# Kernel optimization log

Hardware: AMD Instinct MI355X
Metric: run time of the kernel (lower is better)

The kernel has to match this reference:

```python
import jax, jax.numpy as jnp
import numpy as np

K = 32            # config.k: active latents per token (batch top-k)
THRESHOLD_LR = 0.01
B, S, F = 8, 256, 16384


def setup_inputs() -> dict:
    key = jax.random.key(0)
    k1, k2 = jax.random.split(key)
    x = jax.random.normal(k1, (B, S, F), dtype=jnp.float32)
    token_mask = jax.random.randint(k2, (B, S), 0, 2, dtype=jnp.int32)
    threshold = jnp.zeros((), dtype=jnp.float32)  # persistent EMA buffer, init 0.0
    return {"x": x, "token_mask": token_mask, "threshold": threshold}


def reference(x, token_mask, threshold):
    # Training path of BatchTopKActivationFunction.forward
    b, s, f = x.shape
    num_tokens = b * s
    k_total = K * num_tokens
    neg_min = jnp.finfo(x.dtype).min
    # mask out tokens: x[~token_mask] = finfo.min (so they never enter top-k)
    xm = jnp.where(token_mask.astype(bool)[:, :, None], x, neg_min)
    flat = xm.reshape(-1)                       # [b*s*f]
    vals, idx = jax.lax.top_k(flat, k_total)    # global top-k over flattened tensor
    # scatter relu'd top-k values back into a zero tensor
    result = jnp.zeros_like(flat).at[idx].set(jax.nn.relu(vals)).reshape(b, s, f)
    # EMA threshold update: min of strictly-positive selected values
    pos = vals > 0
    min_pos = jnp.min(jnp.where(pos, vals, jnp.inf))
    new_threshold = jnp.where(
        jnp.any(pos),
        (1.0 - THRESHOLD_LR) * threshold + THRESHOLD_LR * min_pos,
        threshold,
    )
    return result, new_threshold
```

## Files before the change

kernel.cpp:

```cpp
#include <hip/hip_runtime.h>

#define N_ELEMS  33554432
#define N4       8388608
#define N_TOKENS 2048
#define F4       4096
#define K_TOTAL  65536u
#define NBINS    4096

#define C_NG       4096
#define C_WINTH    4097
#define C_CANDTH   4098
#define C_NEED     4099
#define C_FB       4100
#define C_N2       4101
#define C_DONE     4102
#define N_CTR_END  4160

#define GLIST_OFF  8192u
#define CAPG       4194304u
#define LIST2_OFF  (GLIST_OFF + 2u*CAPG)
#define CAP2       4096u
#define FB1_OFF    16777216u
#define CAPF       2097152u
#define FB2_OFF    (FB1_OFF + 2u*CAPF)

#define GBUF 1024
#define GH_BLOCKS 32

__device__ __forceinline__ unsigned keyOf(float f) {
    unsigned b = __float_as_uint(f);
    return b ^ ((unsigned)((int)b >> 31) | 0x80000000u);
}
__device__ __forceinline__ float valOf(unsigned u) {
    unsigned b = (u & 0x80000000u) ? (u ^ 0x80000000u) : ~u;
    return __uint_as_float(b);
}
__device__ __forceinline__ unsigned umaxu(unsigned a, unsigned b) { return a > b ? a : b; }

__global__ void k_init(unsigned* __restrict__ ws) {
    int t = blockIdx.x * 256 + threadIdx.x;
    if (t < N_CTR_END) ws[t] = 0u;
}

__global__ __launch_bounds__(512) void k_stream(const float4* __restrict__ x,
                                                const int* __restrict__ mask,
                                                unsigned* __restrict__ ws,
                                                float4* __restrict__ out) {
    __shared__ uint2 sbuf[GBUF];
    __shared__ unsigned s_cnt, s_base;
    const int tok = blockIdx.x;
    const int tid = threadIdx.x;
    float4* ot = out + (size_t)tok * F4;
    const float4 z = make_float4(0.f, 0.f, 0.f, 0.f);
    if (!mask[tok]) {
        for (int j = tid; j < F4; j += 512) ot[j] = z;
        return;
    }
    if (tid == 0) s_cnt = 0u;
    __syncthreads();
    uint2* glist = (uint2*)(ws + GLIST_OFF);
    const float4* xt = x + (size_t)tok * F4;
    const unsigned baseIdx = (unsigned)tok * 16384u;
    #pragma unroll
    for (int half = 0; half < 2; ++half) {
        const int j0 = tid + half * 2048;
        float4 v0 = xt[j0];
        float4 v1 = xt[j0 + 512];
        float4 v2 = xt[j0 + 1024];
        float4 v3 = xt[j0 + 1536];
        ot[j0] = z; ot[j0 + 512] = z; ot[j0 + 1024] = z; ot[j0 + 1536] = z;
        float fv[16] = {v0.x, v0.y, v0.z, v0.w, v1.x, v1.y, v1.z, v1.w,
                        v2.x, v2.y, v2.z, v2.w, v3.x, v3.y, v3.z, v3.w};
        #pragma unroll
        for (int c = 0; c < 16; ++c) {
            float f = fv[c];
            if (f >= 2.0f) {
                unsigned u = keyOf(f);
                unsigned slot = atomicAdd(&s_cnt, 1u);
                unsigned j = (unsigned)(j0 + (c >> 2) * 512);
                uint2 e = make_uint2(u, baseIdx + j * 4u + (unsigned)(c & 3));
                if (slot < GBUF) sbuf[slot] = e;
                else { unsigned g = atomicAdd(&ws[C_NG], 1u); if (g < CAPG) glist[g] = e; }
            }
        }
    }
    __syncthreads();
    unsigned cnt = s_cnt; if (cnt > GBUF) cnt = GBUF;
    if (tid == 0) s_base = atomicAdd(&ws[C_NG], cnt);
    __syncthreads();
    for (unsigned j = tid; j < cnt; j += 512) {
        unsigned p = s_base + j;
        if (p < CAPG) glist[p] = sbuf[j];
    }
}

__global__ __launch_bounds__(1024) void k_ghist(unsigned* __restrict__ ws) {
    __shared__ unsigned lh[NBINS];
    __shared__ unsigned s_last, s_b1, s_ka, s_found;
    const int t = threadIdx.x;
    for (int b = t; b < NBINS; b += 1024) lh[b] = 0u;
    if (t == 0) s_last = 0u;
    __syncthreads();
    const unsigned ngRaw = ws[C_NG];
    unsigned ng = ngRaw > CAPG ? CAPG : ngRaw;
    const uint2* glist = (const uint2*)(ws + GLIST_OFF);
    for (unsigned i = blockIdx.x * 1024u + (unsigned)t; i < ng; i += GH_BLOCKS * 1024u) {
        unsigned u = glist[i].x;
        unsigned bin = (u - 0xC0000000u) >> 12;
        if (bin > 4095u) bin = 4095u;
        atomicAdd(&lh[bin], 1u);
    }
    __syncthreads();
    for (int b = t; b < NBINS; b += 1024) {
        unsigned c = lh[b];
        if (c) atomicAdd(&ws[b], c);
    }
    __syncthreads();
    if (t == 0) {
        __threadfence();
        unsigned done = atomicAdd(&ws[C_DONE], 1u) + 1u;
        if (done == GH_BLOCKS) s_last = 1u;
    }
    __syncthreads();
    if (!s_last) return;
    unsigned vv[4]; unsigned s = 0u;
    #pragma unroll
    for (int j = 0; j < 4; ++j) {
        vv[j] = __hip_atomic_load(&ws[t * 4 + j], __ATOMIC_RELAXED, __HIP_MEMORY_SCOPE_AGENT);
        s += vv[j];
    }
    unsigned* sc = lh;
    if (t == 0) s_found = 0u;
    sc[t] = s;
    __syncthreads();
    for (int off = 1; off < 1024; off <<= 1) {
        unsigned a = sc[t];
        unsigned b2 = (t + off < 1024) ? sc[t + off] : 0u;
        __syncthreads();
        sc[t] = a + b2;
        __syncthreads();
    }
    unsigned run = (t < 1023) ? sc[t + 1] : 0u;
    #pragma unroll
    for (int j = 3; j >= 0; --j) {
        unsigned prev = run; run += vv[j];
        if (run >= K_TOTAL && prev < K_TOTAL) {
            s_b1 = (unsigned)(t * 4 + j); s_ka = prev; s_found = 1u;
        }
    }
    __syncthreads();
    if (t == 0) {
        unsigned total = sc[0];
        unsigned fb = (s_found == 0u) || (total < K_TOTAL) || (s_b1 == 4095u) || (ngRaw > CAPG);
        ws[C_FB] = fb ? 1u : 0u;
        if (!fb) {
            unsigned candTh = 0xC0000000u + (s_b1 << 12);
            ws[C_CANDTH] = candTh;
            ws[C_WINTH]  = candTh + 0x1000u;
            ws[C_NEED]   = K_TOTAL - s_ka;
        }
    }
}

__global__ __launch_bounds__(256) void k_scatter(unsigned* __restrict__ ws,
                                                 float* __restrict__ out) {
    if (ws[C_FB]) return;
    const unsigned winTh = ws[C_WINTH], candTh = ws[C_CANDTH];
    unsigned ng = ws[C_NG]; if (ng > CAPG) ng = CAPG;
    uint2* glist = (uint2*)(ws + GLIST_OFF);
    uint2* list2 = (uint2*)(ws + LIST2_OFF);
    const unsigned stride = gridDim.x * 256u;
    for (unsigned i = blockIdx.x * 256u + (unsigned)threadIdx.x; i < ng; i += stride) {
        uint2 e = glist[i];
        if (e.x >= winTh) out[e.y] = valOf(e.x);
        else if (e.x >= candTh) {
            unsigned g = atomicAdd(&ws[C_N2], 1u);
            if (g < CAP2) list2[g] = e;
        }
    }
}

__global__ __launch_bounds__(1024) void k_tail(const float4* __restrict__ x,
                                               const int* __restrict__ mask,
                                               unsigned* __restrict__ ws,
                                               float* __restrict__ out,
                                               const float* __restrict__ thr) {
    __shared__ __align__(16) unsigned smem[9216];
    __shared__ unsigned sB1, sKA, sMode, sNegmin, sB2, sNeed, sCnt;
    const int t = threadIdx.x;
    const unsigned rawn2 = ws[C_N2];
    const unsigned fb = ws[C_FB] | (rawn2 > CAP2 ? 1u : 0u);

    if (!fb) {
        uint2* ent = (uint2*)smem;
        unsigned* red = smem + 8192;
        const unsigned n2 = rawn2;
        const unsigned need = ws[C_NEED];
        uint2* list2 = (uint2*)(ws + LIST2_OFF);
        for (unsigned i = (unsigned)t; i < n2; i += 1024u) ent[i] = list2[i];
        __syncthreads();
        unsigned minSel = 0xFFFFFFFFu;
        for (unsigned i = (unsigned)t; i < n2; i += 1024u) {
            uint2 e = ent[i];
            unsigned rank = 0u;
            for (unsigned j = 0; j < n2; ++j) {
                uint2 o = ent[j];
                rank += (o.x > e.x || (o.x == e.x && o.y < e.y)) ? 1u : 0u;
            }
            if (rank < need) {
                out[e.y] = valOf(e.x);
                if (e.x < minSel) minSel = e.x;
            }
        }
        red[t] = minSel;
        __syncthreads();
        for (int off = 512; off > 0; off >>= 1) {
            if (t < off) red[t] = red[t] < red[t + off] ? red[t] : red[t + off];
            __syncthreads();
        }
        if (t == 0) {
            out[N_ELEMS] = 0.99f * thr[0] + 0.01f * valOf(red[0]);
        }
        return;
    }

    unsigned* lh = smem;
    unsigned* sred = smem + 4096;
    for (int b = t; b < NBINS; b += 1024) lh[b] = 0u;
    if (t == 0) sCnt = 0u;
    __syncthreads();
    unsigned negmin = 0u;
    for (int tok = 0; tok < N_TOKENS; ++tok) {
        if (!mask[tok]) continue;
        const float4* xt = x + (size_t)tok * F4;
        for (int j = t; j < F4; j += 1024) {
            float4 v = xt[j];
            float fv[4] = {v.x, v.y, v.z, v.w};
            #pragma unroll
            for (int c = 0; c < 4; ++c) {
                float f = fv[c];
                unsigned u = keyOf(f);
                atomicAdd(&lh[u >> 20], 1u);
                if (f > 0.0f) negmin = umaxu(negmin, ~u);
            }
        }
    }
    __syncthreads();
    sred[t] = negmin; __syncthreads();
    for (int off = 512; off > 0; off >>= 1) {
        if (t < off) sred[t] = umaxu(sred[t], sred[t + off]);
        __syncthreads();
    }
    if (t == 0) {
        sNegmin = sred[0];
        unsigned tot = 0u;
        for (int b = 0; b < NBINS; ++b) tot += lh[b];
        if (tot <= K_TOTAL) sMode = 1u;
        else {
            sMode = 0u;
            unsigned run = 0u, prev = 0u; int b1 = 0;
            for (int b = NBINS - 1; b >= 0; --b) {
                prev = run; run += lh[b];
                if (run >= K_TOTAL && prev < K_TOTAL) { b1 = b; break; }
            }
            sB1 = (unsigned)b1; sKA = prev;
        }
        sCnt = 0u;
    }
    __syncthreads();
    if (sMode == 1u) {
        for (int tok = 0; tok < N_TOKENS; ++tok) {
            if (!mask[tok]) continue;
            const float4* xt = x + (size_t)tok * F4;
            float* ot = out + (size_t)tok * 16384;
            for (int j = t; j < F4; j += 1024) {
                float4 v = xt[j];
                ot[j * 4 + 0] = fmaxf(v.x, 0.f); ot[j * 4 + 1] = fmaxf(v.y, 0.f);
                ot[j * 4 + 2] = fmaxf(v.z, 0.f); ot[j * 4 + 3] = fmaxf(v.w, 0.f);
            }
        }
        if (t == 0) {
            float th = thr[0], newt = th;
            if (sNegmin) newt = 0.99f * th + 0.01f * valOf(~sNegmin);
            out[N_ELEMS] = newt;
        }
        return;
    }
    const unsigned B1c = sB1;
    uint2* fb1 = (uint2*)(ws + FB1_OFF);
    for (int tok = 0; tok < N_TOKENS; ++tok) {
        if (!mask[tok]) continue;
        const float4* xt = x + (size_t)tok * F4;
        const unsigned baseIdx = (unsigned)tok * 16384u;
        for (int j = t; j < F4; j += 1024) {
            float4 v = xt[j];
            float fv[4] = {v.x, v.y, v.z, v.w};
            #pragma unroll
            for (int c = 0; c < 4; ++c) {
                float f = fv[c];
                unsigned u = keyOf(f);
                unsigned p = u >> 20;
                unsigned idx = baseIdx + (unsigned)j * 4u + (unsigned)c;
                if (p > B1c) out[idx] = fmaxf(f, 0.f);
                else if (p == B1c) {
                    unsigned g = atomicAdd(&sCnt, 1u);
                    if (g < CAPF) fb1[g] = make_uint2(u, idx);
                }
            }
        }
    }
    __syncthreads();
    unsigned n1 = sCnt > CAPF ? CAPF : sCnt;
    __syncthreads();
    if (t < 256) lh[t] = 0u;
    if (t == 0) sCnt = 0u;
    __syncthreads();
    for (unsigned i = t; i < n1; i += 1024)
        atomicAdd(&lh[(fb1[i].x >> 12) & 255u], 1u);
    __syncthreads();
    if (t == 0) {
        unsigned run = sKA, prev = sKA; int b2 = 0;
        for (int b = 255; b >= 0; --b) {
            prev = run; run += lh[b];
            if (run >= K_TOTAL) { b2 = b; break; }
        }
        sB2 = (unsigned)b2; sNeed = K_TOTAL - prev;
    }
    __syncthreads();
    const unsigned B2 = sB2, need = sNeed;
    uint2* fb2 = (uint2*)(ws + FB2_OFF);
    for (unsigned i = t; i < n1; i += 1024) {
        uint2 e = fb1[i];
        unsigned bb = (e.x >> 12) & 255u;
        if (bb > B2) out[e.y] = fmaxf(valOf(e.x), 0.f);
        else if (bb == B2) {
            unsigned g = atomicAdd(&sCnt, 1u);
            if (g < CAPF) fb2[g] = e;
        }
    }
    __syncthreads();
    unsigned n2 = sCnt > CAPF ? CAPF : sCnt;
    unsigned minSel = 0xFFFFFFFFu;
    for (unsigned i = t; i < n2; i += 1024) {
        uint2 e = fb2[i];
        unsigned rank = 0u;
        for (unsigned jj = 0; jj < n2; ++jj) {
            uint2 o = fb2[jj];
            rank += (o.x > e.x || (o.x == e.x && o.y < e.y)) ? 1u : 0u;
        }
        if (rank < need) { out[e.y] = fmaxf(valOf(e.x), 0.f); if (e.x < minSel) minSel = e.x; }
    }
    __syncthreads();
    sred[t] = minSel; __syncthreads();
    for (int off = 512; off > 0; off >>= 1) {
        if (t < off) sred[t] = sred[t] < sred[t + off] ? sred[t] : sred[t + off];
        __syncthreads();
    }
    if (t == 0) {
        float th = thr[0], newt = th;
        unsigned vku = sred[0];
        if (vku != 0xFFFFFFFFu) {
            float vk = valOf(vku);
            float minpos; int any;
            if (vk > 0.f) { minpos = vk; any = 1; }
            else { any = (sNegmin != 0u); minpos = any ? valOf(~sNegmin) : 0.f; }
            if (any) newt = 0.99f * th + 0.01f * minpos;
        }
        out[N_ELEMS] = newt;
    }
}

extern "C" void kernel_launch(void* const* d_in, const int* in_sizes, int n_in,
                              void* d_out, int out_size, void* d_ws, size_t ws_size,
                              hipStream_t stream) {
    const float4* x  = (const float4*)d_in[0];
    const int* mask  = (const int*)d_in[1];
    const float* thr = (const float*)d_in[2];
    float* out       = (float*)d_out;
    unsigned* ws     = (unsigned*)d_ws;

    k_init    <<<17, 256, 0, stream>>>(ws);
    k_stream  <<<N_TOKENS, 512, 0, stream>>>(x, mask, ws, (float4*)out);
    k_ghist   <<<GH_BLOCKS, 1024, 0, stream>>>(ws);
    k_scatter <<<256, 256, 0, stream>>>(ws, out);
    k_tail    <<<1, 1024, 0, stream>>>(x, mask, ws, out, thr);
}
```

Baseline: 272.3 us.

## Defer output zeroing to per-token emit kernel using pivot threshold

The streaming pass now only gates candidates and records a per-token segment (base, count) in global memory instead of zeroing the output. A multi-block candidate kernel finds the exact pivot key and index with a last-block rank step. A new per-token emit kernel then zeroes each row and writes the selected values from its own segment, so the final scatter is local to each row rather than random across the whole output. Overflow of the shared buffer now forces the fallback path instead of spilling to the global list. The cost is an extra pass over the output rows and an extra kernel launch.

```diff
diff --git a/kernel.cpp b/kernel.cpp
--- a/kernel.cpp
+++ b/kernel.cpp
@@ -1,7 +1,6 @@
 #include <hip/hip_runtime.h>
 
 #define N_ELEMS  33554432
-#define N4       8388608
 #define N_TOKENS 2048
 #define F4       4096
 #define K_TOTAL  65536u
@@ -14,9 +13,13 @@
 #define C_FB       4100
 #define C_N2       4101
 #define C_DONE     4102
+#define C_PK       4107
+#define C_PIDX     4108
+#define C_DONE2    4109
 #define N_CTR_END  4160
 
-#define GLIST_OFF  8192u
+#define SEG_OFF    4608u
+#define GLIST_OFF  16384u
 #define CAPG       4194304u
 #define LIST2_OFF  (GLIST_OFF + 2u*CAPG)
 #define CAP2       4096u
@@ -26,6 +29,7 @@
 
 #define GBUF 1024
 #define GH_BLOCKS 32
+#define CP_BLOCKS 64
 
 __device__ __forceinline__ unsigned keyOf(float f) {
     unsigned b = __float_as_uint(f);
@@ -42,23 +46,19 @@
     if (t < N_CTR_END) ws[t] = 0u;
 }
 
-__global__ __launch_bounds__(512) void k_stream(const float4* __restrict__ x,
-                                                const int* __restrict__ mask,
-                                                unsigned* __restrict__ ws,
-                                                float4* __restrict__ out) {
+__global__ __launch_bounds__(512) void k_gate(const float4* __restrict__ x,
+                                              const int* __restrict__ mask,
+                                              unsigned* __restrict__ ws) {
     __shared__ uint2 sbuf[GBUF];
     __shared__ unsigned s_cnt, s_base;
     const int tok = blockIdx.x;
     const int tid = threadIdx.x;
-    float4* ot = out + (size_t)tok * F4;
-    const float4 z = make_float4(0.f, 0.f, 0.f, 0.f);
     if (!mask[tok]) {
-        for (int j = tid; j < F4; j += 512) ot[j] = z;
+        if (tid == 0) { ws[SEG_OFF + 2u*tok] = 0u; ws[SEG_OFF + 2u*tok + 1u] = 0u; }
         return;
     }
     if (tid == 0) s_cnt = 0u;
     __syncthreads();
-    uint2* glist = (uint2*)(ws + GLIST_OFF);
     const float4* xt = x + (size_t)tok * F4;
     const unsigned baseIdx = (unsigned)tok * 16384u;
     #pragma unroll
@@ -68,7 +68,6 @@
         float4 v1 = xt[j0 + 512];
         float4 v2 = xt[j0 + 1024];
         float4 v3 = xt[j0 + 1536];
-        ot[j0] = z; ot[j0 + 512] = z; ot[j0 + 1024] = z; ot[j0 + 1536] = z;
         float fv[16] = {v0.x, v0.y, v0.z, v0.w, v1.x, v1.y, v1.z, v1.w,
                         v2.x, v2.y, v2.z, v2.w, v3.x, v3.y, v3.z, v3.w};
         #pragma unroll
@@ -78,18 +77,26 @@
                 unsigned u = keyOf(f);
                 unsigned slot = atomicAdd(&s_cnt, 1u);
                 unsigned j = (unsigned)(j0 + (c >> 2) * 512);
-                uint2 e = make_uint2(u, baseIdx + j * 4u + (unsigned)(c & 3));
-                if (slot < GBUF) sbuf[slot] = e;
-                else { unsigned g = atomicAdd(&ws[C_NG], 1u); if (g < CAPG) glist[g] = e; }
+                if (slot < GBUF) sbuf[slot] = make_uint2(u, baseIdx + j * 4u + (unsigned)(c & 3));
             }
         }
     }
     __syncthreads();
-    unsigned cnt = s_cnt; if (cnt > GBUF) cnt = GBUF;
-    if (tid == 0) s_base = atomicAdd(&ws[C_NG], cnt);
-    __syncthreads();
-    for (unsigned j = tid; j < cnt; j += 512) {
-        unsigned p = s_base + j;
+    unsigned cnt = s_cnt;
+    const bool ovf = cnt > GBUF;
+    if (ovf) cnt = GBUF;
+    if (tid == 0) {
+        unsigned b = atomicAdd(&ws[C_NG], cnt);
+        s_base = b;
+        ws[SEG_OFF + 2u*tok] = b;
+        ws[SEG_OFF + 2u*tok + 1u] = cnt;
+        if (ovf) atomicOr(&ws[C_FB], 1u);
+    }
+    __syncthreads();
+    uint2* glist = (uint2*)(ws + GLIST_OFF);
+    const unsigned b0 = s_base;
+    for (unsigned j = tid; j < cnt; j += 512u) {
+        unsigned p = b0 + j;
         if (p < CAPG) glist[p] = sbuf[j];
     }
 }
@@ -151,8 +158,10 @@
     __syncthreads();
     if (t == 0) {
         unsigned total = sc[0];
-        unsigned fb = (s_found == 0u) || (total < K_TOTAL) || (s_b1 == 4095u) || (ngRaw > CAPG);
-        ws[C_FB] = fb ? 1u : 0u;
+        unsigned prevFB = __hip_atomic_load(&ws[C_FB], __ATOMIC_RELAXED, __HIP_MEMORY_SCOPE_AGENT);
+        unsigned fb = prevFB | ((s_found == 0u) || (total < K_TOTAL) ||
+                                (s_b1 == 4095u) || (ngRaw > CAPG) ? 1u : 0u);
+        ws[C_FB] = fb;
         if (!fb) {
             unsigned candTh = 0xC0000000u + (s_b1 << 12);
             ws[C_CANDTH] = candTh;
@@ -162,70 +171,100 @@
     }
 }
 
-__global__ __launch_bounds__(256) void k_scatter(unsigned* __restrict__ ws,
-                                                 float* __restrict__ out) {
+__global__ __launch_bounds__(256) void k_candpivot(unsigned* __restrict__ ws,
+                                                   float* __restrict__ out,
+                                                   const float* __restrict__ thr) {
+    __shared__ __align__(16) uint2 ent[CAP2];
+    __shared__ unsigned s_last, s_pk, s_pidx;
+    const int t = threadIdx.x;
     if (ws[C_FB]) return;
     const unsigned winTh = ws[C_WINTH], candTh = ws[C_CANDTH];
     unsigned ng = ws[C_NG]; if (ng > CAPG) ng = CAPG;
-    uint2* glist = (uint2*)(ws + GLIST_OFF);
+    const uint2* glist = (const uint2*)(ws + GLIST_OFF);
     uint2* list2 = (uint2*)(ws + LIST2_OFF);
-    const unsigned stride = gridDim.x * 256u;
-    for (unsigned i = blockIdx.x * 256u + (unsigned)threadIdx.x; i < ng; i += stride) {
+    if (t == 0) s_last = 0u;
+    for (unsigned i = blockIdx.x * 256u + (unsigned)t; i < ng; i += CP_BLOCKS * 256u) {
         uint2 e = glist[i];
-        if (e.x >= winTh) out[e.y] = valOf(e.x);
-        else if (e.x >= candTh) {
+        if (e.x >= candTh && e.x < winTh) {
             unsigned g = atomicAdd(&ws[C_N2], 1u);
             if (g < CAP2) list2[g] = e;
         }
     }
-}
-
-__global__ __launch_bounds__(1024) void k_tail(const float4* __restrict__ x,
-                                               const int* __restrict__ mask,
-                                               unsigned* __restrict__ ws,
-                                               float* __restrict__ out,
-                                               const float* __restrict__ thr) {
-    __shared__ __align__(16) unsigned smem[9216];
+    __syncthreads();
+    if (t == 0) {
+        __threadfence();
+        unsigned done = atomicAdd(&ws[C_DONE2], 1u) + 1u;
+        if (done == CP_BLOCKS) s_last = 1u;
+    }
+    __syncthreads();
+    if (!s_last) return;
+    unsigned n2 = __hip_atomic_load(&ws[C_N2], __ATOMIC_RELAXED, __HIP_MEMORY_SCOPE_AGENT);
+    if (n2 > CAP2) { if (t == 0) ws[C_FB] = 1u; return; }
+    const unsigned need = ws[C_NEED];
+    unsigned* l2w = ws + LIST2_OFF;
+    for (unsigned i = (unsigned)t; i < n2; i += 256u) {
+        unsigned kx = __hip_atomic_load(&l2w[2u*i],     __ATOMIC_RELAXED, __HIP_MEMORY_SCOPE_AGENT);
+        unsigned ix = __hip_atomic_load(&l2w[2u*i + 1u], __ATOMIC_RELAXED, __HIP_MEMORY_SCOPE_AGENT);
+        ent[i] = make_uint2(kx, ix);
+    }
+    __syncthreads();
+    for (unsigned i = (unsigned)t; i < n2; i += 256u) {
+        uint2 e = ent[i];
+        unsigned rank = 0u;
+        for (unsigned j = 0; j < n2; ++j) {
+            uint2 o = ent[j];
+            rank += (o.x > e.x || (o.x == e.x && o.y < e.y)) ? 1u : 0u;
+        }
+        if (rank == need - 1u) { s_pk = e.x; s_pidx = e.y; }
+    }
+    __syncthreads();
+    if (t == 0) {
+        ws[C_PK] = s_pk; ws[C_PIDX] = s_pidx;
+        out[N_ELEMS] = 0.99f * thr[0] + 0.01f * valOf(s_pk);
+    }
+}
+
+__global__ __launch_bounds__(512) void k_emit(unsigned* __restrict__ ws,
+                                              float4* __restrict__ out) {
+    __shared__ uint2 ent[GBUF];
+    const int tok = blockIdx.x;
+    const int tid = threadIdx.x;
+    const unsigned fb = ws[C_FB];
+    unsigned cnt = fb ? 0u : ws[SEG_OFF + 2u*tok + 1u];
+    const unsigned base = ws[SEG_OFF + 2u*tok];
+    const unsigned pk   = ws[C_PK];
+    const unsigned pidx = ws[C_PIDX];
+    const uint2* glist = (const uint2*)(ws + GLIST_OFF);
+    for (unsigned i = (unsigned)tid; i < cnt; i += 512u) {
+        unsigned p = base + i;
+        ent[i] = (p < CAPG) ? glist[p] : make_uint2(0u, 0u);
+    }
+    float4* ot = out + (size_t)tok * F4;
+    const float4 z = make_float4(0.f, 0.f, 0.f, 0.f);
+    #pragma unroll
+    for (int half = 0; half < 2; ++half) {
+        const int j0 = tid + half * 2048;
+        ot[j0] = z; ot[j0 + 512] = z; ot[j0 + 1024] = z; ot[j0 + 1536] = z;
+    }
+    __syncthreads();
+    float* of = (float*)out;
+    for (unsigned i = (unsigned)tid; i < cnt; i += 512u) {
+        uint2 e = ent[i];
+        if (e.x > pk || (e.x == pk && e.y <= pidx))
+            of[e.y] = valOf(e.x);
+    }
+}
+
+__global__ __launch_bounds__(1024) void k_fallback(const float4* __restrict__ x,
+                                                   const int* __restrict__ mask,
+                                                   unsigned* __restrict__ ws,
+                                                   float* __restrict__ out,
+                                                   const float* __restrict__ thr) {
+    if (ws[C_FB] == 0u) return;
+    __shared__ unsigned lh[NBINS];
+    __shared__ unsigned sred[1024];
     __shared__ unsigned sB1, sKA, sMode, sNegmin, sB2, sNeed, sCnt;
     const int t = threadIdx.x;
-    const unsigned rawn2 = ws[C_N2];
-    const unsigned fb = ws[C_FB] | (rawn2 > CAP2 ? 1u : 0u);
-
-    if (!fb) {
-        uint2* ent = (uint2*)smem;
-        unsigned* red = smem + 8192;
-        const unsigned n2 = rawn2;
-        const unsigned need = ws[C_NEED];
-        uint2* list2 = (uint2*)(ws + LIST2_OFF);
-        for (unsigned i = (unsigned)t; i < n2; i += 1024u) ent[i] = list2[i];
-        __syncthreads();
-        unsigned minSel = 0xFFFFFFFFu;
-        for (unsigned i = (unsigned)t; i < n2; i += 1024u) {
-            uint2 e = ent[i];
-            unsigned rank = 0u;
-            for (unsigned j = 0; j < n2; ++j) {
-                uint2 o = ent[j];
-                rank += (o.x > e.x || (o.x == e.x && o.y < e.y)) ? 1u : 0u;
-            }
-            if (rank < need) {
-                out[e.y] = valOf(e.x);
-                if (e.x < minSel) minSel = e.x;
-            }
-        }
-        red[t] = minSel;
-        __syncthreads();
-        for (int off = 512; off > 0; off >>= 1) {
-            if (t < off) red[t] = red[t] < red[t + off] ? red[t] : red[t + off];
-            __syncthreads();
-        }
-        if (t == 0) {
-            out[N_ELEMS] = 0.99f * thr[0] + 0.01f * valOf(red[0]);
-        }
-        return;
-    }
-
-    unsigned* lh = smem;
-    unsigned* sred = smem + 4096;
     for (int b = t; b < NBINS; b += 1024) lh[b] = 0u;
     if (t == 0) sCnt = 0u;
     __syncthreads();
@@ -379,9 +418,10 @@
     float* out       = (float*)d_out;
     unsigned* ws     = (unsigned*)d_ws;
 
-    k_init    <<<17, 256, 0, stream>>>(ws);
-    k_stream  <<<N_TOKENS, 512, 0, stream>>>(x, mask, ws, (float4*)out);
-    k_ghist   <<<GH_BLOCKS, 1024, 0, stream>>>(ws);
-    k_scatter <<<256, 256, 0, stream>>>(ws, out);
-    k_tail    <<<1, 1024, 0, stream>>>(x, mask, ws, out, thr);
-}
+    k_init      <<<17, 256, 0, stream>>>(ws);
+    k_gate      <<<N_TOKENS, 512, 0, stream>>>(x, mask, ws);
+    k_ghist     <<<GH_BLOCKS, 1024, 0, stream>>>(ws);
+    k_candpivot <<<CP_BLOCKS, 256, 0, stream>>>(ws, out, thr);
+    k_emit      <<<N_TOKENS, 512, 0, stream>>>(ws, (float4*)out);
+    k_fallback  <<<1, 1024, 0, stream>>>(x, mask, ws, out, thr);
+}
```

Measured after the change: 272.1 us. About the same (-0.1%).

## Fuse histogram into streaming pass and merge scatter with tail selection

Applied to the files above, without the earlier changes.

Builds the 4096-bin key histogram in shared memory inside the per-token streaming kernel, and the last finishing block computes the threshold bin. Candidates now go to fixed per-token segments with per-token counts instead of a global atomic list. The separate scatter and single-block tail kernels become one multi-block kernel whose last block does the exact rank selection. This cuts the kernel count from five to three and drops the histogram re-read of the candidate list. In exchange, per-token buffers that overflow now force the slow fallback path, and shared-memory atomics are added to the streaming loop.

```diff
diff --git a/kernel.cpp b/kernel.cpp
--- a/kernel.cpp
+++ b/kernel.cpp
@@ -1,31 +1,30 @@
 #include <hip/hip_runtime.h>
 
 #define N_ELEMS  33554432
-#define N4       8388608
 #define N_TOKENS 2048
 #define F4       4096
 #define K_TOTAL  65536u
 #define NBINS    4096
 
-#define C_NG       4096
 #define C_WINTH    4097
 #define C_CANDTH   4098
 #define C_NEED     4099
 #define C_FB       4100
 #define C_N2       4101
 #define C_DONE     4102
+#define C_DONE2    4103
 #define N_CTR_END  4160
 
+#define CNT_OFF    4608u
 #define GLIST_OFF  8192u
-#define CAPG       4194304u
-#define LIST2_OFF  (GLIST_OFF + 2u*CAPG)
+#define GBUF       1024u
+#define LIST2_OFF  (GLIST_OFF + 2u*GBUF*N_TOKENS)
 #define CAP2       4096u
 #define FB1_OFF    16777216u
 #define CAPF       2097152u
 #define FB2_OFF    (FB1_OFF + 2u*CAPF)
 
-#define GBUF 1024
-#define GH_BLOCKS 32
+#define FIN_BLOCKS 512
 
 __device__ __forceinline__ unsigned keyOf(float f) {
     unsigned b = __float_as_uint(f);
@@ -36,123 +35,109 @@
     return __uint_as_float(b);
 }
 __device__ __forceinline__ unsigned umaxu(unsigned a, unsigned b) { return a > b ? a : b; }
+__device__ __forceinline__ unsigned aload(const unsigned* p) {
+    return __hip_atomic_load(p, __ATOMIC_RELAXED, __HIP_MEMORY_SCOPE_AGENT);
+}
 
 __global__ void k_init(unsigned* __restrict__ ws) {
     int t = blockIdx.x * 256 + threadIdx.x;
     if (t < N_CTR_END) ws[t] = 0u;
 }
 
-__global__ __launch_bounds__(512) void k_stream(const float4* __restrict__ x,
-                                                const int* __restrict__ mask,
-                                                unsigned* __restrict__ ws,
-                                                float4* __restrict__ out) {
-    __shared__ uint2 sbuf[GBUF];
-    __shared__ unsigned s_cnt, s_base;
+__global__ __launch_bounds__(512) void k_main(const float4* __restrict__ x,
+                                              const int* __restrict__ mask,
+                                              unsigned* __restrict__ ws,
+                                              float4* __restrict__ out) {
+    __shared__ unsigned lh[NBINS];
+    __shared__ unsigned s_cnt, s_flag, s_b1, s_ka, s_found;
     const int tok = blockIdx.x;
     const int tid = threadIdx.x;
+    const bool live = mask[tok] != 0;
     float4* ot = out + (size_t)tok * F4;
     const float4 z = make_float4(0.f, 0.f, 0.f, 0.f);
-    if (!mask[tok]) {
-        for (int j = tid; j < F4; j += 512) ot[j] = z;
-        return;
-    }
+    for (int b = tid; b < NBINS; b += 512) lh[b] = 0u;
     if (tid == 0) s_cnt = 0u;
     __syncthreads();
-    uint2* glist = (uint2*)(ws + GLIST_OFF);
-    const float4* xt = x + (size_t)tok * F4;
-    const unsigned baseIdx = (unsigned)tok * 16384u;
+    uint2* gseg = (uint2*)(ws + GLIST_OFF) + (size_t)tok * GBUF;
+    if (live) {
+        const float4* xt = x + (size_t)tok * F4;
+        const unsigned baseIdx = (unsigned)tok * 16384u;
+        float4 v[8];
+        #pragma unroll
+        for (int k = 0; k < 8; ++k) v[k] = xt[tid + k * 512];
+        #pragma unroll
+        for (int k = 0; k < 8; ++k) ot[tid + k * 512] = z;
+        #pragma unroll
+        for (int k = 0; k < 8; ++k) {
+            const float ff[4] = {v[k].x, v[k].y, v[k].z, v[k].w};
+            #pragma unroll
+            for (int c = 0; c < 4; ++c) {
+                float f = ff[c];
+                if (f >= 2.0f) {
+                    unsigned u = keyOf(f);
+                    unsigned bin = (u - 0xC0000000u) >> 12;
+                    if (bin > 4095u) bin = 4095u;
+                    atomicAdd(&lh[bin], 1u);
+                    unsigned slot = atomicAdd(&s_cnt, 1u);
+                    if (slot < GBUF)
+                        gseg[slot] = make_uint2(u, baseIdx + ((unsigned)tid + (unsigned)k * 512u) * 4u + (unsigned)c);
+                }
+            }
+        }
+    } else {
+        #pragma unroll
+        for (int k = 0; k < 8; ++k) ot[tid + k * 512] = z;
+    }
+    __syncthreads();
+    unsigned cnt = s_cnt;
+    const bool ovf = cnt > GBUF;
+    if (ovf) cnt = GBUF;
+    if (tid == 0) {
+        ws[CNT_OFF + (unsigned)tok] = cnt;
+        if (ovf) atomicOr(&ws[C_FB], 1u);
+    }
+    if (live) {
+        for (int b = tid; b < NBINS; b += 512) {
+            unsigned c = lh[b];
+            if (c) atomicAdd(&ws[b], c);
+        }
+    }
+    __syncthreads();
+    if (tid == 0) {
+        __threadfence();
+        unsigned d = atomicAdd(&ws[C_DONE], 1u);
+        s_flag = (d == (unsigned)(N_TOKENS - 1)) ? 1u : 0u;
+    }
+    __syncthreads();
+    if (!s_flag) return;
+    unsigned vv[8]; unsigned s = 0u;
     #pragma unroll
-    for (int half = 0; half < 2; ++half) {
-        const int j0 = tid + half * 2048;
-        float4 v0 = xt[j0];
-        float4 v1 = xt[j0 + 512];
-        float4 v2 = xt[j0 + 1024];
-        float4 v3 = xt[j0 + 1536];
-        ot[j0] = z; ot[j0 + 512] = z; ot[j0 + 1024] = z; ot[j0 + 1536] = z;
-        float fv[16] = {v0.x, v0.y, v0.z, v0.w, v1.x, v1.y, v1.z, v1.w,
-                        v2.x, v2.y, v2.z, v2.w, v3.x, v3.y, v3.z, v3.w};
-        #pragma unroll
-        for (int c = 0; c < 16; ++c) {
-            float f = fv[c];
-            if (f >= 2.0f) {
-                unsigned u = keyOf(f);
-                unsigned slot = atomicAdd(&s_cnt, 1u);
-                unsigned j = (unsigned)(j0 + (c >> 2) * 512);
-                uint2 e = make_uint2(u, baseIdx + j * 4u + (unsigned)(c & 3));
-                if (slot < GBUF) sbuf[slot] = e;
-                else { unsigned g = atomicAdd(&ws[C_NG], 1u); if (g < CAPG) glist[g] = e; }
-            }
-        }
-    }
-    __syncthreads();
-    unsigned cnt = s_cnt; if (cnt > GBUF) cnt = GBUF;
-    if (tid == 0) s_base = atomicAdd(&ws[C_NG], cnt);
-    __syncthreads();
-    for (unsigned j = tid; j < cnt; j += 512) {
-        unsigned p = s_base + j;
-        if (p < CAPG) glist[p] = sbuf[j];
-    }
-}
-
-__global__ __launch_bounds__(1024) void k_ghist(unsigned* __restrict__ ws) {
-    __shared__ unsigned lh[NBINS];
-    __shared__ unsigned s_last, s_b1, s_ka, s_found;
-    const int t = threadIdx.x;
-    for (int b = t; b < NBINS; b += 1024) lh[b] = 0u;
-    if (t == 0) s_last = 0u;
-    __syncthreads();
-    const unsigned ngRaw = ws[C_NG];
-    unsigned ng = ngRaw > CAPG ? CAPG : ngRaw;
-    const uint2* glist = (const uint2*)(ws + GLIST_OFF);
-    for (unsigned i = blockIdx.x * 1024u + (unsigned)t; i < ng; i += GH_BLOCKS * 1024u) {
-        unsigned u = glist[i].x;
-        unsigned bin = (u - 0xC0000000u) >> 12;
-        if (bin > 4095u) bin = 4095u;
-        atomicAdd(&lh[bin], 1u);
-    }
-    __syncthreads();
-    for (int b = t; b < NBINS; b += 1024) {
-        unsigned c = lh[b];
-        if (c) atomicAdd(&ws[b], c);
-    }
-    __syncthreads();
-    if (t == 0) {
-        __threadfence();
-        unsigned done = atomicAdd(&ws[C_DONE], 1u) + 1u;
-        if (done == GH_BLOCKS) s_last = 1u;
-    }
-    __syncthreads();
-    if (!s_last) return;
-    unsigned vv[4]; unsigned s = 0u;
+    for (int j = 0; j < 8; ++j) { vv[j] = aload(&ws[tid * 8 + j]); s += vv[j]; }
+    unsigned* sc = lh;
+    if (tid == 0) s_found = 0u;
+    sc[tid] = s;
+    __syncthreads();
+    for (int off = 1; off < 512; off <<= 1) {
+        unsigned a = sc[tid];
+        unsigned b2 = (tid + off < 512) ? sc[tid + off] : 0u;
+        __syncthreads();
+        sc[tid] = a + b2;
+        __syncthreads();
+    }
+    unsigned run = (tid < 511) ? sc[tid + 1] : 0u;
     #pragma unroll
-    for (int j = 0; j < 4; ++j) {
-        vv[j] = __hip_atomic_load(&ws[t * 4 + j], __ATOMIC_RELAXED, __HIP_MEMORY_SCOPE_AGENT);
-        s += vv[j];
-    }
-    unsigned* sc = lh;
-    if (t == 0) s_found = 0u;
-    sc[t] = s;
-    __syncthreads();
-    for (int off = 1; off < 1024; off <<= 1) {
-        unsigned a = sc[t];
-        unsigned b2 = (t + off < 1024) ? sc[t + off] : 0u;
-        __syncthreads();
-        sc[t] = a + b2;
-        __syncthreads();
-    }
-    unsigned run = (t < 1023) ? sc[t + 1] : 0u;
-    #pragma unroll
-    for (int j = 3; j >= 0; --j) {
+    for (int j = 7; j >= 0; --j) {
         unsigned prev = run; run += vv[j];
         if (run >= K_TOTAL && prev < K_TOTAL) {
-            s_b1 = (unsigned)(t * 4 + j); s_ka = prev; s_found = 1u;
-        }
-    }
-    __syncthreads();
-    if (t == 0) {
+            s_b1 = (unsigned)(tid * 8 + j); s_ka = prev; s_found = 1u;
+        }
+    }
+    __syncthreads();
+    if (tid == 0) {
         unsigned total = sc[0];
-        unsigned fb = (s_found == 0u) || (total < K_TOTAL) || (s_b1 == 4095u) || (ngRaw > CAPG);
-        ws[C_FB] = fb ? 1u : 0u;
+        unsigned prevFB = aload(&ws[C_FB]);
+        unsigned fb = prevFB | (((s_found == 0u) || (total < K_TOTAL) || (s_b1 == 4095u)) ? 1u : 0u);
+        ws[C_FB] = fb;
         if (!fb) {
             unsigned candTh = 0xC0000000u + (s_b1 << 12);
             ws[C_CANDTH] = candTh;
@@ -162,45 +147,51 @@
     }
 }
 
-__global__ __launch_bounds__(256) void k_scatter(unsigned* __restrict__ ws,
-                                                 float* __restrict__ out) {
-    if (ws[C_FB]) return;
-    const unsigned winTh = ws[C_WINTH], candTh = ws[C_CANDTH];
-    unsigned ng = ws[C_NG]; if (ng > CAPG) ng = CAPG;
-    uint2* glist = (uint2*)(ws + GLIST_OFF);
-    uint2* list2 = (uint2*)(ws + LIST2_OFF);
-    const unsigned stride = gridDim.x * 256u;
-    for (unsigned i = blockIdx.x * 256u + (unsigned)threadIdx.x; i < ng; i += stride) {
-        uint2 e = glist[i];
-        if (e.x >= winTh) out[e.y] = valOf(e.x);
-        else if (e.x >= candTh) {
-            unsigned g = atomicAdd(&ws[C_N2], 1u);
-            if (g < CAP2) list2[g] = e;
-        }
-    }
-}
-
-__global__ __launch_bounds__(1024) void k_tail(const float4* __restrict__ x,
-                                               const int* __restrict__ mask,
-                                               unsigned* __restrict__ ws,
-                                               float* __restrict__ out,
-                                               const float* __restrict__ thr) {
-    __shared__ __align__(16) unsigned smem[9216];
+__global__ __launch_bounds__(512) void k_finish(const float4* __restrict__ x,
+                                                const int* __restrict__ mask,
+                                                unsigned* __restrict__ ws,
+                                                float* __restrict__ out,
+                                                const float* __restrict__ thr) {
+    __shared__ __align__(16) unsigned smem[8192];
+    __shared__ unsigned s_last, s_pk;
     __shared__ unsigned sB1, sKA, sMode, sNegmin, sB2, sNeed, sCnt;
     const int t = threadIdx.x;
-    const unsigned rawn2 = ws[C_N2];
-    const unsigned fb = ws[C_FB] | (rawn2 > CAP2 ? 1u : 0u);
-
-    if (!fb) {
+    const unsigned fb0 = ws[C_FB];
+    if (!fb0) {
+        const unsigned winTh = ws[C_WINTH], candTh = ws[C_CANDTH];
+        const uint2* glist = (const uint2*)(ws + GLIST_OFF);
+        uint2* list2 = (uint2*)(ws + LIST2_OFF);
+        for (unsigned tok = blockIdx.x; tok < N_TOKENS; tok += FIN_BLOCKS) {
+            const unsigned cnt = ws[CNT_OFF + tok];
+            const uint2* gseg = glist + (size_t)tok * GBUF;
+            for (unsigned i = (unsigned)t; i < cnt; i += 512u) {
+                uint2 e = gseg[i];
+                if (e.x >= winTh) out[e.y] = valOf(e.x);
+                else if (e.x >= candTh) {
+                    unsigned g = atomicAdd(&ws[C_N2], 1u);
+                    if (g < CAP2) list2[g] = e;
+                }
+            }
+        }
+    }
+    __syncthreads();
+    if (t == 0) {
+        __threadfence();
+        unsigned d = atomicAdd(&ws[C_DONE2], 1u);
+        s_last = (d == FIN_BLOCKS - 1u) ? 1u : 0u;
+    }
+    __syncthreads();
+    if (!s_last) return;
+
+    const unsigned n2 = aload(&ws[C_N2]);
+    if (!fb0 && n2 <= CAP2) {
         uint2* ent = (uint2*)smem;
-        unsigned* red = smem + 8192;
-        const unsigned n2 = rawn2;
         const unsigned need = ws[C_NEED];
-        uint2* list2 = (uint2*)(ws + LIST2_OFF);
-        for (unsigned i = (unsigned)t; i < n2; i += 1024u) ent[i] = list2[i];
-        __syncthreads();
-        unsigned minSel = 0xFFFFFFFFu;
-        for (unsigned i = (unsigned)t; i < n2; i += 1024u) {
+        const unsigned* l2w = ws + LIST2_OFF;
+        for (unsigned i = (unsigned)t; i < n2; i += 512u)
+            ent[i] = make_uint2(aload(&l2w[2u*i]), aload(&l2w[2u*i + 1u]));
+        __syncthreads();
+        for (unsigned i = (unsigned)t; i < n2; i += 512u) {
             uint2 e = ent[i];
             unsigned rank = 0u;
             for (unsigned j = 0; j < n2; ++j) {
@@ -209,31 +200,24 @@
             }
             if (rank < need) {
                 out[e.y] = valOf(e.x);
-                if (e.x < minSel) minSel = e.x;
-            }
-        }
-        red[t] = minSel;
-        __syncthreads();
-        for (int off = 512; off > 0; off >>= 1) {
-            if (t < off) red[t] = red[t] < red[t + off] ? red[t] : red[t + off];
-            __syncthreads();
-        }
-        if (t == 0) {
-            out[N_ELEMS] = 0.99f * thr[0] + 0.01f * valOf(red[0]);
-        }
+                if (rank == need - 1u) s_pk = e.x;
+            }
+        }
+        __syncthreads();
+        if (t == 0) out[N_ELEMS] = 0.99f * thr[0] + 0.01f * valOf(s_pk);
         return;
     }
 
     unsigned* lh = smem;
     unsigned* sred = smem + 4096;
-    for (int b = t; b < NBINS; b += 1024) lh[b] = 0u;
+    for (int b = t; b < NBINS; b += 512) lh[b] = 0u;
     if (t == 0) sCnt = 0u;
     __syncthreads();
     unsigned negmin = 0u;
     for (int tok = 0; tok < N_TOKENS; ++tok) {
         if (!mask[tok]) continue;
         const float4* xt = x + (size_t)tok * F4;
-        for (int j = t; j < F4; j += 1024) {
+        for (int j = t; j < F4; j += 512) {
             float4 v = xt[j];
             float fv[4] = {v.x, v.y, v.z, v.w};
             #pragma unroll
@@ -246,8 +230,9 @@
         }
     }
     __syncthreads();
+    sred[t & 511] = 0u;  __syncthreads();
     sred[t] = negmin; __syncthreads();
-    for (int off = 512; off > 0; off >>= 1) {
+    for (int off = 256; off > 0; off >>= 1) {
         if (t < off) sred[t] = umaxu(sred[t], sred[t + off]);
         __syncthreads();
     }
@@ -273,7 +258,7 @@
             if (!mask[tok]) continue;
             const float4* xt = x + (size_t)tok * F4;
             float* ot = out + (size_t)tok * 16384;
-            for (int j = t; j < F4; j += 1024) {
+            for (int j = t; j < F4; j += 512) {
                 float4 v = xt[j];
                 ot[j * 4 + 0] = fmaxf(v.x, 0.f); ot[j * 4 + 1] = fmaxf(v.y, 0.f);
                 ot[j * 4 + 2] = fmaxf(v.z, 0.f); ot[j * 4 + 3] = fmaxf(v.w, 0.f);
@@ -292,7 +277,7 @@
         if (!mask[tok]) continue;
         const float4* xt = x + (size_t)tok * F4;
         const unsigned baseIdx = (unsigned)tok * 16384u;
-        for (int j = t; j < F4; j += 1024) {
+        for (int j = t; j < F4; j += 512) {
             float4 v = xt[j];
             float fv[4] = {v.x, v.y, v.z, v.w};
             #pragma unroll
@@ -315,7 +300,7 @@
     if (t < 256) lh[t] = 0u;
     if (t == 0) sCnt = 0u;
     __syncthreads();
-    for (unsigned i = t; i < n1; i += 1024)
+    for (unsigned i = t; i < n1; i += 512)
         atomicAdd(&lh[(fb1[i].x >> 12) & 255u], 1u);
     __syncthreads();
     if (t == 0) {
@@ -329,7 +314,7 @@
     __syncthreads();
     const unsigned B2 = sB2, need = sNeed;
     uint2* fb2 = (uint2*)(ws + FB2_OFF);
-    for (unsigned i = t; i < n1; i += 1024) {
+    for (unsigned i = t; i < n1; i += 512) {
         uint2 e = fb1[i];
         unsigned bb = (e.x >> 12) & 255u;
         if (bb > B2) out[e.y] = fmaxf(valOf(e.x), 0.f);
@@ -339,12 +324,12 @@
         }
     }
     __syncthreads();
-    unsigned n2 = sCnt > CAPF ? CAPF : sCnt;
+    unsigned n2f = sCnt > CAPF ? CAPF : sCnt;
     unsigned minSel = 0xFFFFFFFFu;
-    for (unsigned i = t; i < n2; i += 1024) {
+    for (unsigned i = t; i < n2f; i += 512) {
         uint2 e = fb2[i];
         unsigned rank = 0u;
-        for (unsigned jj = 0; jj < n2; ++jj) {
+        for (unsigned jj = 0; jj < n2f; ++jj) {
             uint2 o = fb2[jj];
             rank += (o.x > e.x || (o.x == e.x && o.y < e.y)) ? 1u : 0u;
         }
@@ -352,7 +337,7 @@
     }
     __syncthreads();
     sred[t] = minSel; __syncthreads();
-    for (int off = 512; off > 0; off >>= 1) {
+    for (int off = 256; off > 0; off >>= 1) {
         if (t < off) sred[t] = sred[t] < sred[t + off] ? sred[t] : sred[t + off];
         __syncthreads();
     }
@@ -379,9 +364,7 @@
     float* out       = (float*)d_out;
     unsigned* ws     = (unsigned*)d_ws;
 
-    k_init    <<<17, 256, 0, stream>>>(ws);
-    k_stream  <<<N_TOKENS, 512, 0, stream>>>(x, mask, ws, (float4*)out);
-    k_ghist   <<<GH_BLOCKS, 1024, 0, stream>>>(ws);
-    k_scatter <<<256, 256, 0, stream>>>(ws, out);
-    k_tail    <<<1, 1024, 0, stream>>>(x, mask, ws, out, thr);
-}
+    k_init   <<<17, 256, 0, stream>>>(ws);
+    k_main   <<<N_TOKENS, 512, 0, stream>>>(x, mask, ws, (float4*)out);
+    k_finish <<<FIN_BLOCKS, 512, 0, stream>>>(x, mask, ws, out, thr);
+}
```

Measured after the change: 403.3 us. 48.1% more time.

## Fuse histogram into streaming pass and split output zeroing into separate blocks

Applied to the files above, without the earlier changes.

Each live-token block now builds its candidate histogram in shared memory as it streams x and merges it into the global bins. The last block to finish, detected through a done counter, runs the prefix scan to find the threshold bin, which removes the k_ghist launch and the re-read of the candidate list. Zeroing the output moves into dedicated fill blocks interleaved with the token blocks, and the scatter grid is doubled. This adds shared-memory atomics to the hot loop and a serial last-block tail.

```diff
diff --git a/kernel.cpp b/kernel.cpp
--- a/kernel.cpp
+++ b/kernel.cpp
@@ -25,7 +25,8 @@
 #define FB2_OFF    (FB1_OFF + 2u*CAPF)
 
 #define GBUF 1024
-#define GH_BLOCKS 32
+#define FILL_BLOCKS 1024
+#define STREAM_BLOCKS (N_TOKENS + FILL_BLOCKS)
 
 __device__ __forceinline__ unsigned keyOf(float f) {
     unsigned b = __float_as_uint(f);
@@ -36,6 +37,9 @@
     return __uint_as_float(b);
 }
 __device__ __forceinline__ unsigned umaxu(unsigned a, unsigned b) { return a > b ? a : b; }
+__device__ __forceinline__ unsigned aload(const unsigned* p) {
+    return __hip_atomic_load(p, __ATOMIC_RELAXED, __HIP_MEMORY_SCOPE_AGENT);
+}
 
 __global__ void k_init(unsigned* __restrict__ ws) {
     int t = blockIdx.x * 256 + threadIdx.x;
@@ -46,113 +50,104 @@
                                                 const int* __restrict__ mask,
                                                 unsigned* __restrict__ ws,
                                                 float4* __restrict__ out) {
+    __shared__ unsigned lh[NBINS];
     __shared__ uint2 sbuf[GBUF];
-    __shared__ unsigned s_cnt, s_base;
-    const int tok = blockIdx.x;
+    __shared__ unsigned s_cnt, s_base, s_flag, s_found, s_b1, s_ka;
+    const int b = blockIdx.x;
     const int tid = threadIdx.x;
-    float4* ot = out + (size_t)tok * F4;
-    const float4 z = make_float4(0.f, 0.f, 0.f, 0.f);
-    if (!mask[tok]) {
-        for (int j = tid; j < F4; j += 512) ot[j] = z;
+    const int r = b % 3;
+    if (r == 2) {
+        const int fid = b / 3;
+        float4* o = out + (size_t)fid * 8192;
+        const float4 z = make_float4(0.f, 0.f, 0.f, 0.f);
+        #pragma unroll
+        for (int k = 0; k < 16; ++k) o[tid + k * 512] = z;
         return;
     }
+    const int tok = (b / 3) * 2 + r;
+    const bool live = mask[tok] != 0;
+    uint2* glist = (uint2*)(ws + GLIST_OFF);
     if (tid == 0) s_cnt = 0u;
-    __syncthreads();
-    uint2* glist = (uint2*)(ws + GLIST_OFF);
-    const float4* xt = x + (size_t)tok * F4;
-    const unsigned baseIdx = (unsigned)tok * 16384u;
+    if (live) {
+        for (int bb = tid; bb < NBINS; bb += 512) lh[bb] = 0u;
+        __syncthreads();
+        const float4* xt = x + (size_t)tok * F4;
+        const unsigned baseIdx = (unsigned)tok * 16384u;
+        #pragma unroll
+        for (int half = 0; half < 2; ++half) {
+            const int j0 = tid + half * 2048;
+            float4 v0 = xt[j0];
+            float4 v1 = xt[j0 + 512];
+            float4 v2 = xt[j0 + 1024];
+            float4 v3 = xt[j0 + 1536];
+            float fv[16] = {v0.x, v0.y, v0.z, v0.w, v1.x, v1.y, v1.z, v1.w,
+                            v2.x, v2.y, v2.z, v2.w, v3.x, v3.y, v3.z, v3.w};
+            #pragma unroll
+            for (int c = 0; c < 16; ++c) {
+                float f = fv[c];
+                if (f >= 2.0f) {
+                    unsigned u = keyOf(f);
+                    unsigned bin = (u - 0xC0000000u) >> 12;
+                    if (bin > 4095u) bin = 4095u;
+                    atomicAdd(&lh[bin], 1u);
+                    unsigned slot = atomicAdd(&s_cnt, 1u);
+                    unsigned j = (unsigned)(j0 + (c >> 2) * 512);
+                    uint2 e = make_uint2(u, baseIdx + j * 4u + (unsigned)(c & 3));
+                    if (slot < GBUF) sbuf[slot] = e;
+                    else { unsigned g = atomicAdd(&ws[C_NG], 1u); if (g < CAPG) glist[g] = e; }
+                }
+            }
+        }
+        __syncthreads();
+        for (int bb = tid; bb < NBINS; bb += 512) {
+            unsigned c = lh[bb];
+            if (c) atomicAdd(&ws[bb], c);
+        }
+        unsigned cnt = s_cnt; if (cnt > GBUF) cnt = GBUF;
+        if (tid == 0) s_base = atomicAdd(&ws[C_NG], cnt);
+        __syncthreads();
+        for (unsigned j = tid; j < cnt; j += 512u) {
+            unsigned p = s_base + j;
+            if (p < CAPG) glist[p] = sbuf[j];
+        }
+    }
+    __syncthreads();
+    if (tid == 0) {
+        __threadfence();
+        unsigned d = atomicAdd(&ws[C_DONE], 1u);
+        s_flag = (d == (unsigned)(N_TOKENS - 1)) ? 1u : 0u;
+        s_found = 0u;
+    }
+    __syncthreads();
+    if (!s_flag) return;
+    unsigned vv[8]; unsigned s = 0u;
     #pragma unroll
-    for (int half = 0; half < 2; ++half) {
-        const int j0 = tid + half * 2048;
-        float4 v0 = xt[j0];
-        float4 v1 = xt[j0 + 512];
-        float4 v2 = xt[j0 + 1024];
-        float4 v3 = xt[j0 + 1536];
-        ot[j0] = z; ot[j0 + 512] = z; ot[j0 + 1024] = z; ot[j0 + 1536] = z;
-        float fv[16] = {v0.x, v0.y, v0.z, v0.w, v1.x, v1.y, v1.z, v1.w,
-                        v2.x, v2.y, v2.z, v2.w, v3.x, v3.y, v3.z, v3.w};
-        #pragma unroll
-        for (int c = 0; c < 16; ++c) {
-            float f = fv[c];
-            if (f >= 2.0f) {
-                unsigned u = keyOf(f);
-                unsigned slot = atomicAdd(&s_cnt, 1u);
-                unsigned j = (unsigned)(j0 + (c >> 2) * 512);
-                uint2 e = make_uint2(u, baseIdx + j * 4u + (unsigned)(c & 3));
-                if (slot < GBUF) sbuf[slot] = e;
-                else { unsigned g = atomicAdd(&ws[C_NG], 1u); if (g < CAPG) glist[g] = e; }
-            }
-        }
-    }
-    __syncthreads();
-    unsigned cnt = s_cnt; if (cnt > GBUF) cnt = GBUF;
-    if (tid == 0) s_base = atomicAdd(&ws[C_NG], cnt);
-    __syncthreads();
-    for (unsigned j = tid; j < cnt; j += 512) {
-        unsigned p = s_base + j;
-        if (p < CAPG) glist[p] = sbuf[j];
-    }
-}
-
-__global__ __launch_bounds__(1024) void k_ghist(unsigned* __restrict__ ws) {
-    __shared__ unsigned lh[NBINS];
-    __shared__ unsigned s_last, s_b1, s_ka, s_found;
-    const int t = threadIdx.x;
-    for (int b = t; b < NBINS; b += 1024) lh[b] = 0u;
-    if (t == 0) s_last = 0u;
-    __syncthreads();
-    const unsigned ngRaw = ws[C_NG];
-    unsigned ng = ngRaw > CAPG ? CAPG : ngRaw;
-    const uint2* glist = (const uint2*)(ws + GLIST_OFF);
-    for (unsigned i = blockIdx.x * 1024u + (unsigned)t; i < ng; i += GH_BLOCKS * 1024u) {
-        unsigned u = glist[i].x;
-        unsigned bin = (u - 0xC0000000u) >> 12;
-        if (bin > 4095u) bin = 4095u;
-        atomicAdd(&lh[bin], 1u);
-    }
-    __syncthreads();
-    for (int b = t; b < NBINS; b += 1024) {
-        unsigned c = lh[b];
-        if (c) atomicAdd(&ws[b], c);
-    }
-    __syncthreads();
-    if (t == 0) {
-        __threadfence();
-        unsigned done = atomicAdd(&ws[C_DONE], 1u) + 1u;
-        if (done == GH_BLOCKS) s_last = 1u;
-    }
-    __syncthreads();
-    if (!s_last) return;
-    unsigned vv[4]; unsigned s = 0u;
+    for (int j = 0; j < 8; ++j) { vv[j] = aload(&ws[tid * 8 + j]); s += vv[j]; }
+    unsigned* sc = lh;
+    sc[tid] = s;
+    __syncthreads();
+    for (int off = 1; off < 512; off <<= 1) {
+        unsigned a = sc[tid];
+        unsigned b2 = (tid + off < 512) ? sc[tid + off] : 0u;
+        __syncthreads();
+        sc[tid] = a + b2;
+        __syncthreads();
+    }
+    unsigned run = (tid < 511) ? sc[tid + 1] : 0u;
     #pragma unroll
-    for (int j = 0; j < 4; ++j) {
-        vv[j] = __hip_atomic_load(&ws[t * 4 + j], __ATOMIC_RELAXED, __HIP_MEMORY_SCOPE_AGENT);
-        s += vv[j];
-    }
-    unsigned* sc = lh;
-    if (t == 0) s_found = 0u;
-    sc[t] = s;
-    __syncthreads();
-    for (int off = 1; off < 1024; off <<= 1) {
-        unsigned a = sc[t];
-        unsigned b2 = (t + off < 1024) ? sc[t + off] : 0u;
-        __syncthreads();
-        sc[t] = a + b2;
-        __syncthreads();
-    }
-    unsigned run = (t < 1023) ? sc[t + 1] : 0u;
-    #pragma unroll
-    for (int j = 3; j >= 0; --j) {
+    for (int j = 7; j >= 0; --j) {
         unsigned prev = run; run += vv[j];
         if (run >= K_TOTAL && prev < K_TOTAL) {
-            s_b1 = (unsigned)(t * 4 + j); s_ka = prev; s_found = 1u;
-        }
-    }
-    __syncthreads();
-    if (t == 0) {
+            s_b1 = (unsigned)(tid * 8 + j); s_ka = prev; s_found = 1u;
+        }
+    }
+    __syncthreads();
+    if (tid == 0) {
         unsigned total = sc[0];
-        unsigned fb = (s_found == 0u) || (total < K_TOTAL) || (s_b1 == 4095u) || (ngRaw > CAPG);
-        ws[C_FB] = fb ? 1u : 0u;
+        unsigned ngRaw = aload(&ws[C_NG]);
+        unsigned fb = ((s_found == 0u) || (total < K_TOTAL) ||
+                       (s_b1 == 4095u) || (ngRaw > CAPG)) ? 1u : 0u;
+        ws[C_FB] = fb;
         if (!fb) {
             unsigned candTh = 0xC0000000u + (s_b1 << 12);
             ws[C_CANDTH] = candTh;
@@ -339,12 +334,12 @@
         }
     }
     __syncthreads();
-    unsigned n2 = sCnt > CAPF ? CAPF : sCnt;
+    unsigned n2f = sCnt > CAPF ? CAPF : sCnt;
     unsigned minSel = 0xFFFFFFFFu;
-    for (unsigned i = t; i < n2; i += 1024) {
+    for (unsigned i = t; i < n2f; i += 1024) {
         uint2 e = fb2[i];
         unsigned rank = 0u;
-        for (unsigned jj = 0; jj < n2; ++jj) {
+        for (unsigned jj = 0; jj < n2f; ++jj) {
             uint2 o = fb2[jj];
             rank += (o.x > e.x || (o.x == e.x && o.y < e.y)) ? 1u : 0u;
         }
@@ -380,8 +375,7 @@
     unsigned* ws     = (unsigned*)d_ws;
 
     k_init    <<<17, 256, 0, stream>>>(ws);
-    k_stream  <<<N_TOKENS, 512, 0, stream>>>(x, mask, ws, (float4*)out);
-    k_ghist   <<<GH_BLOCKS, 1024, 0, stream>>>(ws);
-    k_scatter <<<256, 256, 0, stream>>>(ws, out);
+    k_stream  <<<STREAM_BLOCKS, 512, 0, stream>>>(x, mask, ws, (float4*)out);
+    k_scatter <<<512, 256, 0, stream>>>(ws, out);
     k_tail    <<<1, 1024, 0, stream>>>(x, mask, ws, out, thr);
 }
```

Measured after the change: 381.9 us. +40.3%, slower.
